# Kernel tuning notes

Hardware: AMD Instinct MI355X
Metric: run time of the kernel (lower is better)

## Reference

```python
import jax, jax.numpy as jnp
import numpy as np

Q_STEPS, Q_TOKENS = 16, 64
KV_STEPS, KV_TOKENS = 64, 64
WINDOW = 2
TOPK = 32
DIM = 512
BATCH = 8
NUM_CONTEXTS = 2


def build_local_mask(q_steps, q_tokens, kv_steps, kv_tokens, window):
    # centers: nearest kv step for each query step
    centers = np.round(np.linspace(0, kv_steps - 1, q_steps)).astype(np.int64)
    steps = np.arange(kv_steps)
    allowed = np.abs(steps[None, :] - centers[:, None]) <= window  # [q_steps, kv_steps]
    allowed = np.repeat(np.repeat(allowed, q_tokens, axis=0), kv_tokens, axis=1)
    return jnp.where(jnp.asarray(allowed), 0.0, -jnp.inf).astype(jnp.float32)


MASK = build_local_mask(Q_STEPS, Q_TOKENS, KV_STEPS, KV_TOKENS, WINDOW)


def setup_inputs() -> dict:
    key = jax.random.key(0)
    ks = jax.random.split(key, 12)
    s = 1.0 / np.sqrt(DIM)
    return {
        "query": jax.random.normal(ks[0], (BATCH, Q_STEPS, Q_TOKENS, DIM), jnp.float32),
        "source": jax.random.normal(ks[1], (BATCH, KV_STEPS, KV_TOKENS, DIM), jnp.float32),
        "ctx1": jax.random.normal(ks[2], (BATCH, DIM), jnp.float32),
        "ctx2": jax.random.normal(ks[3], (BATCH, DIM), jnp.float32),
        "Wq": jax.random.normal(ks[4], (DIM, DIM), jnp.float32) * s,
        "bq": jnp.zeros((DIM,), jnp.float32),
        "Wk": jax.random.normal(ks[5], (DIM, DIM), jnp.float32) * s,
        "bk": jnp.zeros((DIM,), jnp.float32),
        "Wv": jax.random.normal(ks[6], (DIM, DIM), jnp.float32) * s,
        "bv": jnp.zeros((DIM,), jnp.float32),
        "Wo": jax.random.normal(ks[7], (DIM, DIM), jnp.float32) * s,
        "bo": jnp.zeros((DIM,), jnp.float32),
        "Wc": jax.random.normal(ks[8], (NUM_CONTEXTS * DIM, 2 * DIM), jnp.float32) * s,
        "bc": jnp.zeros((2 * DIM,), jnp.float32),
    }


def reference(query, source, ctx1, ctx2, Wq, bq, Wk, bk, Wv, bv, Wo, bo, Wc, bc):
    B = query.shape[0]
    # CrossScaleCondition: fuse contexts -> per-batch FiLM params gamma, beta [B, dim]
    fused = jnp.concatenate([ctx1, ctx2], axis=-1)          # [B, num_contexts*dim]
    gb = fused @ Wc + bc                                     # [B, 2*dim]
    gamma, beta = jnp.split(gb, 2, axis=-1)

    q_flat = query.reshape(B, Q_STEPS * Q_TOKENS, DIM)       # [B, Lq, d]
    src_flat = source.reshape(B, KV_STEPS * KV_TOKENS, DIM)  # [B, Lkv, d]

    q_mod = q_flat * (1.0 + gamma[:, None, :]) + beta[:, None, :]
    q = q_mod @ Wq + bq
    k = src_flat @ Wk + bk
    v = src_flat @ Wv + bv

    scores = jnp.einsum('bqd,bkd->bqk', q, k) / jnp.sqrt(jnp.float32(DIM))
    scores = scores + MASK[None]                             # local window mask

    topk_scores, topk_idx = jax.lax.top_k(scores, TOPK)      # [B, Lq, k]
    selected_v = jax.vmap(lambda vb, ib: vb[ib])(v, topk_idx)  # [B, Lq, k, d]

    attn = jax.nn.softmax(topk_scores, axis=-1)
    out = jnp.einsum('bqk,bqkd->bqd', attn, selected_v)
    out = out @ Wo + bo
    return out.reshape(B, Q_STEPS, Q_TOKENS, DIM)
```

## Files before the change

### kernel.cpp

```cpp
#include <hip/hip_runtime.h>

#define NWIN 320
#define SCORE_SCALE 0.04419417382415922f

__constant__ int CENTERS[16] = {0,4,8,13,17,21,25,29,34,38,42,46,50,55,59,63};

typedef __attribute__((ext_vector_type(8))) short v8s;
typedef __attribute__((ext_vector_type(4))) float v4f;

__device__ __forceinline__ float bflo(unsigned u) { return __uint_as_float(u << 16); }
__device__ __forceinline__ float bfhi(unsigned u) { return __uint_as_float(u & 0xffff0000u); }
__device__ __forceinline__ float bf2f(unsigned short h) { return __uint_as_float(((unsigned)h) << 16); }
__device__ __forceinline__ unsigned short f2bf(float x) {
  unsigned u = __float_as_uint(x);
  unsigned r = 0x7fffu + ((u >> 16) & 1u);
  return (unsigned short)((u + r) >> 16);
}

__device__ __forceinline__ int t64_off(int r, int k) {
  return ((r & 31) << 7) + (((((r >> 5) << 2) | (k >> 3)) ^ (r & 7)) << 4) + ((k & 7) << 1);
}
__device__ __forceinline__ int frag_off(int r, int g) {
  return ((r & 31) << 7) + (((((r >> 5) << 2) | g) ^ (r & 7)) << 4);
}

__device__ __forceinline__ void gload_lds16(const void* g, void* l) {
  __builtin_amdgcn_global_load_lds((const __attribute__((address_space(1))) unsigned int*)g,
                                   (__attribute__((address_space(3))) unsigned int*)l, 16, 0, 0);
}

__device__ __forceinline__ void cvt8pair(float4 a, float4 b, uint4& hi4, uint4& lo4) {
  float v[8] = {a.x, a.y, a.z, a.w, b.x, b.y, b.z, b.w};
  unsigned short h[8], l[8];
  #pragma unroll
  for (int e = 0; e < 8; ++e) {
    h[e] = f2bf(v[e]);
    l[e] = f2bf(v[e] - bf2f(h[e]));
  }
  hi4.x = (unsigned)h[0] | ((unsigned)h[1] << 16);
  hi4.y = (unsigned)h[2] | ((unsigned)h[3] << 16);
  hi4.z = (unsigned)h[4] | ((unsigned)h[5] << 16);
  hi4.w = (unsigned)h[6] | ((unsigned)h[7] << 16);
  lo4.x = (unsigned)l[0] | ((unsigned)l[1] << 16);
  lo4.y = (unsigned)l[2] | ((unsigned)l[3] << 16);
  lo4.z = (unsigned)l[4] | ((unsigned)l[5] << 16);
  lo4.w = (unsigned)l[6] | ((unsigned)l[7] << 16);
}

__device__ __forceinline__ uint4 cvt8hi(float4 a, float4 b) {
  uint4 r;
  r.x = (unsigned)f2bf(a.x) | ((unsigned)f2bf(a.y) << 16);
  r.y = (unsigned)f2bf(a.z) | ((unsigned)f2bf(a.w) << 16);
  r.z = (unsigned)f2bf(b.x) | ((unsigned)f2bf(b.y) << 16);
  r.w = (unsigned)f2bf(b.z) | ((unsigned)f2bf(b.w) << 16);
  return r;
}

__device__ __forceinline__ uint2 cvt4(float4 a) {
  uint2 r;
  r.x = (unsigned)f2bf(a.x) | ((unsigned)f2bf(a.y) << 16);
  r.y = (unsigned)f2bf(a.z) | ((unsigned)f2bf(a.w) << 16);
  return r;
}

__global__ __launch_bounds__(256) void prep1_kernel(
    const float* __restrict__ ctx1, const float* __restrict__ ctx2,
    const float* __restrict__ Wc,  float* __restrict__ part,
    const float* __restrict__ Wk,  const float* __restrict__ bq, float* __restrict__ u,
    const float* __restrict__ Wq,
    unsigned short* __restrict__ Wqh, unsigned short* __restrict__ Wql,
    unsigned short* __restrict__ Wkh, unsigned short* __restrict__ Wkl,
    const float* __restrict__ Wv, const float* __restrict__ Wo,
    unsigned short* __restrict__ Wvt, unsigned short* __restrict__ Wot)
{
  __shared__ char img[32768];
  const int bid = blockIdx.x;
  const int tid = threadIdx.x;

  if (bid < 256) {
    const int b = bid >> 5, sl = (bid >> 2) & 7, jq = bid & 3;
    const int j = jq * 256 + tid;
    const int i0 = sl * 128;
    float acc = 0.f;
    #pragma unroll 4
    for (int t = 0; t < 128; ++t) {
      const int i = i0 + t;
      const float f = (i < 512) ? ctx1[b * 512 + i] : ctx2[b * 512 + i - 512];
      acc = fmaf(f, Wc[(size_t)i * 1024 + j], acc);
    }
    part[(b * 8 + sl) * 1024 + j] = acc;
  } else if (bid < 384) {
    const int d = (bid - 256) * 4 + (tid >> 6);
    const int lane = tid & 63;
    float4 a0 = *(const float4*)&Wk[(size_t)d * 512 + lane * 8];
    float4 a1 = *(const float4*)&Wk[(size_t)d * 512 + lane * 8 + 4];
    float4 c0 = *(const float4*)&bq[lane * 8];
    float4 c1 = *(const float4*)&bq[lane * 8 + 4];
    float s = a0.x*c0.x + a0.y*c0.y + a0.z*c0.z + a0.w*c0.w
            + a1.x*c1.x + a1.y*c1.y + a1.z*c1.z + a1.w*c1.w;
    #pragma unroll
    for (int off = 32; off > 0; off >>= 1) s += __shfl_xor(s, off, 64);
    if (lane == 0) u[d] = s * SCORE_SCALE;
  } else if (bid < 640) {
    const int b = bid - 384;
    const int mat = b >> 7;
    const float* Wsrc = mat ? Wk : Wq;
    unsigned short* Wh = mat ? Wkh : Wqh;
    unsigned short* Wl = mat ? Wkl : Wql;
    const size_t e0 = (((size_t)(b & 127) * 256) + tid) * 8;
    float4 x0 = *(const float4*)&Wsrc[e0];
    float4 x1 = *(const float4*)&Wsrc[e0 + 4];
    uint4 h4, l4;
    cvt8pair(x0, x1, h4, l4);
    *(uint4*)&Wh[e0] = h4;
    *(uint4*)&Wl[e0] = l4;
  } else {
    const int cb = bid - 640;
    const int ktile = cb & 15;
    const int mat   = cb >> 4;
    const float* W = mat ? Wo : Wv;
    unsigned short* Dt = mat ? Wot : Wvt;
    const int k  = tid >> 3;
    const int nt = tid & 7;
    #pragma unroll
    for (int e4 = 0; e4 < 16; ++e4) {
      float4 w = *(const float4*)&W[(size_t)(ktile * 32 + k) * 512 + nt * 64 + e4 * 4];
      float vv[4] = {w.x, w.y, w.z, w.w};
      #pragma unroll
      for (int c = 0; c < 4; ++c) {
        const int n = e4 * 4 + c;
        *(unsigned short*)(img + nt * 4096 + t64_off(n, k)) = f2bf(vv[c]);
      }
    }
    __syncthreads();
    const uint4* src = (const uint4*)img;
    uint4* dst = (uint4*)((char*)Dt + (size_t)ktile * 32768);
    for (int i = tid; i < 2048; i += 256) dst[i] = src[i];
  }
}

__global__ __launch_bounds__(256) void prep2_kernel(
    const unsigned short* __restrict__ Wqh, const unsigned short* __restrict__ Wql,
    const unsigned short* __restrict__ Wkh, const unsigned short* __restrict__ Wkl,
    unsigned short* __restrict__ Gt,
    const float* __restrict__ part, const float* __restrict__ bc,
    float* __restrict__ gb)
{
  const int bid = blockIdx.x;
  const int tid = threadIdx.x;

  if (bid < 256) {
    const int lane = tid & 63, l15 = lane & 15, g = lane >> 4;
    const int wave = tid >> 6;
    const int t  = (bid << 2) | wave;
    const int ti = t >> 5, tj = t & 31;
    const int ib = ti << 4, jb = tj << 4;
    const size_t arow = (size_t)(ib + l15) * 512 + (g << 3);
    const size_t brow = (size_t)(jb + l15) * 512 + (g << 3);

    v4f acc = (v4f){0.f, 0.f, 0.f, 0.f};
    #pragma unroll 4
    for (int kk = 0; kk < 16; ++kk) {
      const int kd = kk * 32;
      const v8s ah = *(const v8s*)&Wqh[arow + kd];
      const v8s al = *(const v8s*)&Wql[arow + kd];
      const v8s bh = *(const v8s*)&Wkh[brow + kd];
      const v8s bl = *(const v8s*)&Wkl[brow + kd];
      acc = __builtin_amdgcn_mfma_f32_16x16x32_bf16(ah, bh, acc, 0, 0, 0);
      acc = __builtin_amdgcn_mfma_f32_16x16x32_bf16(al, bh, acc, 0, 0, 0);
      acc = __builtin_amdgcn_mfma_f32_16x16x32_bf16(ah, bl, acc, 0, 0, 0);
    }
    #pragma unroll
    for (int k = 0; k < 4; ++k) {
      const int gi = ib + (g << 2) + k;
      const int gj = jb + l15;
      const float v = acc[k] * SCORE_SCALE;
      const unsigned short hi = f2bf(v);
      const unsigned short lo = f2bf(v - bf2f(hi));
      const int toff = t64_off(gj & 63, gi & 31);
      *(unsigned short*)((char*)Gt + ((size_t)((gi >> 5) * 8 + (gj >> 6)) << 12) + toff) = hi;
      *(unsigned short*)((char*)Gt + ((size_t)(((gi >> 5) + 16) * 8 + (gj >> 6)) << 12) + toff) = lo;
    }
  } else {
    const int rb = bid - 256;
    const int b = rb >> 2, jq = rb & 3;
    const int j = jq * 256 + tid;
    float acc = bc[j];
    #pragma unroll
    for (int sl = 0; sl < 8; ++sl) acc += part[(b * 8 + sl) * 1024 + j];
    gb[b * 1024 + j] = acc;
  }
}

__global__ __launch_bounds__(256) void proj_split(
    const float* __restrict__ A, const unsigned short* __restrict__ Bt,
    const float* __restrict__ bias, const float* __restrict__ gb,
    unsigned short* __restrict__ Qgt)
{
  __shared__ char smem[49152];
  const int tid  = threadIdx.x;
  const int lane = tid & 63, l15 = lane & 15, g = lane >> 4;
  const int wave = tid >> 6, wm = wave >> 1, wn = wave & 1;
  const int bid = blockIdx.x;
  const int xcd = bid & 7, idx = bid >> 3;
  const int mBlk = (idx & 15) | (xcd << 4);
  const int nBlk = idx >> 4;

  const int sr = tid >> 2;
  const int sq = tid & 3;
  const size_t arow = (size_t)(mBlk * 64 + sr) * 512 + sq * 8;
  const int gbbase = ((mBlk >> 4) * 1024) + sq * 8;
  const int awoff = t64_off(sr, sq * 8);

  int aoff[2], boff[4];
  #pragma unroll
  for (int fm = 0; fm < 2; ++fm) aoff[fm] = frag_off(wm * 32 + fm * 16 + l15, g);
  #pragma unroll
  for (int fn = 0; fn < 4; ++fn) {
    const int n = wn * 64 + fn * 16 + l15;
    boff[fn] = ((n >> 6) << 12) + frag_off(n & 63, g);
  }

  v4f acc[2][4];
  #pragma unroll
  for (int fm = 0; fm < 2; ++fm)
    #pragma unroll
    for (int fn = 0; fn < 4; ++fn) acc[fm][fn] = (v4f){0.f, 0.f, 0.f, 0.f};

  auto stageB = [&](int buf, int tk) {
    const char* gsh = (const char*)Bt + ((size_t)(tk * 8 + nBlk * 2) << 12) + (size_t)tid * 16;
    const char* gsl = (const char*)Bt + ((size_t)((tk + 16) * 8 + nBlk * 2) << 12) + (size_t)tid * 16;
    char* dh = smem + buf * 24576 + 8192 + (wave << 10);
    char* dl = smem + buf * 24576 + 16384 + (wave << 10);
    #pragma unroll
    for (int i = 0; i < 2; ++i) {
      gload_lds16(gsh + i * 4096, dh + i * 4096);
      gload_lds16(gsl + i * 4096, dl + i * 4096);
    }
  };
  auto loadA = [&](int tk, float4* r) {
    const int kd = tk * 32;
    r[0] = *(const float4*)&A[arow + kd];
    r[1] = *(const float4*)&A[arow + kd + 4];
    r[2] = *(const float4*)&gb[gbbase + kd];
    r[3] = *(const float4*)&gb[gbbase + kd + 4];
    r[4] = *(const float4*)&gb[gbbase + 512 + kd];
    r[5] = *(const float4*)&gb[gbbase + 512 + kd + 4];
  };
  auto writeA = [&](int buf, float4* r) {
    float4 x0 = r[0], x1 = r[1];
    x0.x = fmaf(x0.x, 1.f + r[2].x, r[4].x); x0.y = fmaf(x0.y, 1.f + r[2].y, r[4].y);
    x0.z = fmaf(x0.z, 1.f + r[2].z, r[4].z); x0.w = fmaf(x0.w, 1.f + r[2].w, r[4].w);
    x1.x = fmaf(x1.x, 1.f + r[3].x, r[5].x); x1.y = fmaf(x1.y, 1.f + r[3].y, r[5].y);
    x1.z = fmaf(x1.z, 1.f + r[3].z, r[5].z); x1.w = fmaf(x1.w, 1.f + r[3].w, r[5].w);
    uint4 hi4, lo4;
    cvt8pair(x0, x1, hi4, lo4);
    *(uint4*)(smem + buf * 24576 + awoff) = hi4;
    *(uint4*)(smem + buf * 24576 + 4096 + awoff) = lo4;
  };

  float4 pr[6];
  stageB(0, 0);
  loadA(0, pr);
  writeA(0, pr);
  __syncthreads();

  for (int tk = 0; tk < 16; ++tk) {
    const int cur = tk & 1;
    if (tk < 15) {
      stageB(cur ^ 1, tk + 1);
      loadA(tk + 1, pr);
    }
    const char* base = smem + cur * 24576;
    const v8s ah0 = *(const v8s*)(base + aoff[0]);
    const v8s ah1 = *(const v8s*)(base + aoff[1]);
    const v8s al0 = *(const v8s*)(base + 4096 + aoff[0]);
    const v8s al1 = *(const v8s*)(base + 4096 + aoff[1]);
    #pragma unroll
    for (int fn = 0; fn < 4; ++fn) {
      const v8s bh = *(const v8s*)(base + 8192 + boff[fn]);
      const v8s bl = *(const v8s*)(base + 16384 + boff[fn]);
      acc[0][fn] = __builtin_amdgcn_mfma_f32_16x16x32_bf16(ah0, bh, acc[0][fn], 0, 0, 0);
      acc[1][fn] = __builtin_amdgcn_mfma_f32_16x16x32_bf16(ah1, bh, acc[1][fn], 0, 0, 0);
      acc[0][fn] = __builtin_amdgcn_mfma_f32_16x16x32_bf16(al0, bh, acc[0][fn], 0, 0, 0);
      acc[1][fn] = __builtin_amdgcn_mfma_f32_16x16x32_bf16(al1, bh, acc[1][fn], 0, 0, 0);
      acc[0][fn] = __builtin_amdgcn_mfma_f32_16x16x32_bf16(ah0, bl, acc[0][fn], 0, 0, 0);
      acc[1][fn] = __builtin_amdgcn_mfma_f32_16x16x32_bf16(ah1, bl, acc[1][fn], 0, 0, 0);
    }
    if (tk < 15) writeA(cur ^ 1, pr);
    __syncthreads();
  }

  #pragma unroll
  for (int fn = 0; fn < 4; ++fn) {
    const int col = nBlk * 128 + wn * 64 + fn * 16 + l15;
    const float bv = bias[col];
    const int kt = col >> 5;
    const int kk = col & 31;
    #pragma unroll
    for (int fm = 0; fm < 2; ++fm) {
      const int r0 = wm * 32 + fm * 16 + g * 4;
      #pragma unroll
      for (int k = 0; k < 4; ++k) {
        const float vv = acc[fm][fn][k] + bv;
        const unsigned short hi = f2bf(vv);
        const unsigned short lo = f2bf(vv - bf2f(hi));
        const int toff = t64_off(r0 + k, kk);
        *(unsigned short*)((char*)Qgt + ((size_t)(kt * 128 + mBlk) << 12) + toff) = hi;
        *(unsigned short*)((char*)Qgt + ((size_t)((kt + 16) * 128 + mBlk) << 12) + toff) = lo;
      }
    }
  }
}

__global__ __launch_bounds__(512) void proj_v(
    const float* __restrict__ A, const unsigned short* __restrict__ Bt,
    const float* __restrict__ bias, unsigned short* __restrict__ Cb)
{
  __shared__ char smem[8192 + 65536];
  char* const LA = smem;
  char* const LB = smem + 8192;

  const int tid  = threadIdx.x;
  const int lane = tid & 63, l15 = lane & 15, g = lane >> 4;
  const int wave = tid >> 6, wm = wave >> 2, wn = wave & 3;
  const int mBlk = blockIdx.x;

  const int sr  = tid >> 3;
  const int sq4 = tid & 7;
  const size_t arow = (size_t)(mBlk * 64 + sr) * 512 + sq4 * 4;
  const int awoff = t64_off(sr, sq4 * 4);

  int aoff[2], boff[8];
  #pragma unroll
  for (int fm = 0; fm < 2; ++fm) aoff[fm] = frag_off(wm * 32 + fm * 16 + l15, g);
  #pragma unroll
  for (int fn = 0; fn < 8; ++fn) {
    const int n = wn * 128 + fn * 16 + l15;
    boff[fn] = ((n >> 6) << 12) + frag_off(n & 63, g);
  }

  v4f acc[2][8];
  #pragma unroll
  for (int fm = 0; fm < 2; ++fm)
    #pragma unroll
    for (int fn = 0; fn < 8; ++fn) acc[fm][fn] = (v4f){0.f, 0.f, 0.f, 0.f};

  auto stageB = [&](int buf, int tk) {
    const char* gs = (const char*)Bt + ((size_t)tk << 15) + (wave << 12) + (lane << 4);
    char* ld = LB + (buf << 15) + (wave << 12);
    #pragma unroll
    for (int i = 0; i < 4; ++i) gload_lds16(gs + (i << 10), ld + (i << 10));
  };

  float4 xa = *(const float4*)&A[arow];
  stageB(0, 0);
  *(uint2*)(LA + awoff) = cvt4(xa);
  __syncthreads();

  for (int tk = 0; tk < 16; ++tk) {
    const int cur = tk & 1;
    if (tk < 15) {
      stageB(cur ^ 1, tk + 1);
      xa = *(const float4*)&A[arow + (tk + 1) * 32];
    }
    const v8s a0 = *(const v8s*)(LA + (cur << 12) + aoff[0]);
    const v8s a1 = *(const v8s*)(LA + (cur << 12) + aoff[1]);
    #pragma unroll
    for (int fn = 0; fn < 8; ++fn) {
      const v8s bb = *(const v8s*)(LB + (cur << 15) + boff[fn]);
      acc[0][fn] = __builtin_amdgcn_mfma_f32_16x16x32_bf16(a0, bb, acc[0][fn], 0, 0, 0);
      acc[1][fn] = __builtin_amdgcn_mfma_f32_16x16x32_bf16(a1, bb, acc[1][fn], 0, 0, 0);
    }
    if (tk < 15) *(uint2*)(LA + ((cur ^ 1) << 12) + awoff) = cvt4(xa);
    __syncthreads();
  }

  #pragma unroll
  for (int fn = 0; fn < 8; ++fn) {
    const int col = wn * 128 + fn * 16 + l15;
    const float bv = bias[col];
    #pragma unroll
    for (int fm = 0; fm < 2; ++fm) {
      const int r0 = mBlk * 64 + wm * 32 + fm * 16 + g * 4;
      #pragma unroll
      for (int k = 0; k < 4; ++k)
        Cb[(size_t)(r0 + k) * 512 + col] = f2bf(acc[fm][fn][k] + bv);
    }
  }
}

__global__ __launch_bounds__(256) void proj_o(
    const float* __restrict__ A, const unsigned short* __restrict__ Bt,
    const float* __restrict__ bias, float* __restrict__ Cf)
{
  __shared__ char smem[24576];
  const int tid  = threadIdx.x;
  const int lane = tid & 63, l15 = lane & 15, g = lane >> 4;
  const int wave = tid >> 6, wm = wave >> 1, wn = wave & 1;
  const int bid = blockIdx.x;
  const int xcd = bid & 7, idx = bid >> 3;
  const int mBlk = (idx & 15) | (xcd << 4);
  const int nBlk = idx >> 4;

  const int sr = tid >> 2;
  const int sq = tid & 3;
  const size_t arow = (size_t)(mBlk * 64 + sr) * 512 + sq * 8;
  const int awoff = t64_off(sr, sq * 8);

  int aoff[2], boff[4];
  #pragma unroll
  for (int fm = 0; fm < 2; ++fm) aoff[fm] = frag_off(wm * 32 + fm * 16 + l15, g);
  #pragma unroll
  for (int fn = 0; fn < 4; ++fn) {
    const int n = wn * 64 + fn * 16 + l15;
    boff[fn] = ((n >> 6) << 12) + frag_off(n & 63, g);
  }

  v4f acc[2][4];
  #pragma unroll
  for (int fm = 0; fm < 2; ++fm)
    #pragma unroll
    for (int fn = 0; fn < 4; ++fn) acc[fm][fn] = (v4f){0.f, 0.f, 0.f, 0.f};

  auto stageB = [&](int buf, int tk) {
    const char* gs = (const char*)Bt + ((size_t)tk << 15) + ((size_t)nBlk << 13) + (size_t)tid * 16;
    char* ld = smem + buf * 12288 + 4096 + (wave << 10);
    #pragma unroll
    for (int i = 0; i < 2; ++i)
      gload_lds16(gs + i * 4096, ld + i * 4096);
  };

  float4 x0 = *(const float4*)&A[arow];
  float4 x1 = *(const float4*)&A[arow + 4];
  stageB(0, 0);
  *(uint4*)(smem + awoff) = cvt8hi(x0, x1);
  __syncthreads();

  for (int tk = 0; tk < 16; ++tk) {
    const int cur = tk & 1;
    if (tk < 15) {
      stageB(cur ^ 1, tk + 1);
      x0 = *(const float4*)&A[arow + (tk + 1) * 32];
      x1 = *(const float4*)&A[arow + (tk + 1) * 32 + 4];
    }
    const char* base = smem + cur * 12288;
    const v8s a0 = *(const v8s*)(base + aoff[0]);
    const v8s a1 = *(const v8s*)(base + aoff[1]);
    #pragma unroll
    for (int fn = 0; fn < 4; ++fn) {
      const v8s bb = *(const v8s*)(base + 4096 + boff[fn]);
      acc[0][fn] = __builtin_amdgcn_mfma_f32_16x16x32_bf16(a0, bb, acc[0][fn], 0, 0, 0);
      acc[1][fn] = __builtin_amdgcn_mfma_f32_16x16x32_bf16(a1, bb, acc[1][fn], 0, 0, 0);
    }
    if (tk < 15) *(uint4*)(smem + (cur ^ 1) * 12288 + awoff) = cvt8hi(x0, x1);
    __syncthreads();
  }

  #pragma unroll
  for (int fn = 0; fn < 4; ++fn) {
    const int col = nBlk * 128 + wn * 64 + fn * 16 + l15;
    const float bv = bias[col];
    #pragma unroll
    for (int fm = 0; fm < 2; ++fm) {
      const int r0 = mBlk * 64 + wm * 32 + fm * 16 + g * 4;
      #pragma unroll
      for (int k = 0; k < 4; ++k)
        Cf[(size_t)(r0 + k) * 512 + col] = acc[fm][fn][k] + bv;
    }
  }
}

__global__ __launch_bounds__(256) void scores_mfma(
    const unsigned short* __restrict__ Qgt, const float* __restrict__ SRC,
    float* __restrict__ S)
{
  const int bs = blockIdx.y;
  const int s = bs & 15, b = bs >> 4;
  const int c  = CENTERS[s];
  const int lo = (c - 2 > 0) ? c - 2 : 0;
  const int hi = (c + 2 < 63) ? c + 2 : 63;
  if ((int)blockIdx.x > hi - lo) return;

  __shared__ char smem[16384];
  char* const LAh = smem;
  char* const LAl = smem + 4096;
  char* const LBh = smem + 8192;
  char* const LBl = smem + 12288;

  const int tid = threadIdx.x;
  const int lane = tid & 63, l15 = lane & 15, g = lane >> 4;
  const int wave = tid >> 6, wm = wave >> 1, wn = wave & 1;
  const int kvrow0 = (b << 12) + ((lo + (int)blockIdx.x) << 6);
  const int qbase  = bs << 6;
  const int sr = tid >> 2, sq = tid & 3;
  const size_t krow = (size_t)(kvrow0 + sr) * 512 + sq * 8;
  const int awoff = t64_off(sr, sq * 8);

  int aoff[2], boff[2];
  #pragma unroll
  for (int f = 0; f < 2; ++f) {
    aoff[f] = frag_off(wm * 32 + f * 16 + l15, g);
    boff[f] = frag_off(wn * 32 + f * 16 + l15, g);
  }

  v4f acc[2][2];
  #pragma unroll
  for (int i = 0; i < 2; ++i)
    #pragma unroll
    for (int j = 0; j < 2; ++j) acc[i][j] = (v4f){0.f, 0.f, 0.f, 0.f};

  for (int tk = 0; tk < 16; ++tk) {
    const int kd = tk * 32;
    {
      const char* gah = (const char*)Qgt + ((size_t)(tk * 128 + bs) << 12) + (size_t)tid * 16;
      const char* gal = (const char*)Qgt + ((size_t)((tk + 16) * 128 + bs) << 12) + (size_t)tid * 16;
      gload_lds16(gah, LAh + (wave << 10));
      gload_lds16(gal, LAl + (wave << 10));
    }
    {
      float4 y0 = *(const float4*)&SRC[krow + kd];
      float4 y1 = *(const float4*)&SRC[krow + kd + 4];
      uint4 bhi, blo;
      cvt8pair(y0, y1, bhi, blo);
      *(uint4*)(LBh + awoff) = bhi;
      *(uint4*)(LBl + awoff) = blo;
    }
    __syncthreads();
    const v8s a0h = *(const v8s*)(LAh + aoff[0]);
    const v8s a1h = *(const v8s*)(LAh + aoff[1]);
    const v8s a0l = *(const v8s*)(LAl + aoff[0]);
    const v8s a1l = *(const v8s*)(LAl + aoff[1]);
    const v8s b0h = *(const v8s*)(LBh + boff[0]);
    const v8s b1h = *(const v8s*)(LBh + boff[1]);
    const v8s b0l = *(const v8s*)(LBl + boff[0]);
    const v8s b1l = *(const v8s*)(LBl + boff[1]);
    acc[0][0] = __builtin_amdgcn_mfma_f32_16x16x32_bf16(a0h, b0h, acc[0][0], 0, 0, 0);
    acc[0][1] = __builtin_amdgcn_mfma_f32_16x16x32_bf16(a0h, b1h, acc[0][1], 0, 0, 0);
    acc[1][0] = __builtin_amdgcn_mfma_f32_16x16x32_bf16(a1h, b0h, acc[1][0], 0, 0, 0);
    acc[1][1] = __builtin_amdgcn_mfma_f32_16x16x32_bf16(a1h, b1h, acc[1][1], 0, 0, 0);
    acc[0][0] = __builtin_amdgcn_mfma_f32_16x16x32_bf16(a0l, b0h, acc[0][0], 0, 0, 0);
    acc[0][1] = __builtin_amdgcn_mfma_f32_16x16x32_bf16(a0l, b1h, acc[0][1], 0, 0, 0);
    acc[1][0] = __builtin_amdgcn_mfma_f32_16x16x32_bf16(a1l, b0h, acc[1][0], 0, 0, 0);
    acc[1][1] = __builtin_amdgcn_mfma_f32_16x16x32_bf16(a1l, b1h, acc[1][1], 0, 0, 0);
    acc[0][0] = __builtin_amdgcn_mfma_f32_16x16x32_bf16(a0h, b0l, acc[0][0], 0, 0, 0);
    acc[0][1] = __builtin_amdgcn_mfma_f32_16x16x32_bf16(a0h, b1l, acc[0][1], 0, 0, 0);
    acc[1][0] = __builtin_amdgcn_mfma_f32_16x16x32_bf16(a1h, b0l, acc[1][0], 0, 0, 0);
    acc[1][1] = __builtin_amdgcn_mfma_f32_16x16x32_bf16(a1h, b1l, acc[1][1], 0, 0, 0);
    __syncthreads();
  }

  #pragma unroll
  for (int fn = 0; fn < 2; ++fn) {
    const int cl = wn * 32 + fn * 16 + l15;
    const int colS = ((int)blockIdx.x << 6) + cl;
    #pragma unroll
    for (int fm = 0; fm < 2; ++fm) {
      const int r0 = qbase + wm * 32 + fm * 16 + g * 4;
      #pragma unroll
      for (int k = 0; k < 4; ++k)
        S[(size_t)(r0 + k) * NWIN + colS] = acc[fm][fn][k];
    }
  }
}

__global__ __launch_bounds__(256) void topk_pv(
    const float* __restrict__ S, const unsigned short* __restrict__ Vb,
    float* __restrict__ O)
{
  __shared__ int   sel_i[4][32];
  __shared__ float sel_p[4][32];

  const int lane = threadIdx.x & 63;
  const int wv   = threadIdx.x >> 6;
  const int b0   = blockIdx.x;
  const int grp  = (b0 & 7) + ((b0 >> 7) << 3);
  const int blk  = (b0 >> 3) & 15;
  const int row  = (((grp << 4) + blk) << 2) + wv;
  const int b    = row >> 10;
  const int s    = (row >> 6) & 15;
  const int c    = CENTERS[s];
  const int lo   = (c - 2 > 0) ? c - 2 : 0;
  const int hi   = (c + 2 < 63) ? c + 2 : 63;
  const int L    = (hi - lo + 1) << 6;
  const size_t vbase = ((size_t)b << 12) + ((size_t)lo << 6);

  const float* srow = S + (size_t)row * NWIN;
  float f[5]; unsigned uo[5];
  #pragma unroll
  for (int j = 0; j < 5; ++j) {
    const int idx = lane + (j << 6);
    const float v = (idx < L) ? srow[idx] : -__builtin_inff();
    f[j] = v;
    const unsigned fb = __float_as_uint(v);
    uo[j] = (fb & 0x80000000u) ? ~fb : (fb | 0x80000000u);
  }

  float m = f[0];
  #pragma unroll
  for (int j = 1; j < 5; ++j) m = fmaxf(m, f[j]);
  #pragma unroll
  for (int off = 32; off > 0; off >>= 1) m = fmaxf(m, __shfl_xor(m, off, 64));

  unsigned T = 0u;
  for (int bit = 31; bit >= 0; --bit) {
    const unsigned cand = T | (1u << bit);
    int cnt = 0;
    #pragma unroll
    for (int j = 0; j < 5; ++j)
      cnt += __popcll(__ballot(uo[j] >= cand));
    if (cnt >= 32) T = cand;
  }

  int base = 0;
  #pragma unroll
  for (int j = 0; j < 5; ++j) {
    const unsigned long long gm = __ballot(uo[j] > T);
    if (uo[j] > T) {
      const int rank = base + __builtin_amdgcn_mbcnt_hi(
          (unsigned)(gm >> 32), __builtin_amdgcn_mbcnt_lo((unsigned)gm, 0));
      sel_i[wv][rank] = lane + (j << 6);
      sel_p[wv][rank] = __expf(f[j] - m);
    }
    base += __popcll(gm);
  }
  #pragma unroll
  for (int j = 0; j < 5; ++j) {
    const unsigned long long em = __ballot(uo[j] == T);
    if (uo[j] == T) {
      const int er = base + __builtin_amdgcn_mbcnt_hi(
          (unsigned)(em >> 32), __builtin_amdgcn_mbcnt_lo((unsigned)em, 0));
      if (er < 32) {
        sel_i[wv][er] = lane + (j << 6);
        sel_p[wv][er] = __expf(f[j] - m);
      }
    }
    base += __popcll(em);
  }

  asm volatile("s_waitcnt lgkmcnt(0)" ::: "memory");

  const int   si = sel_i[wv][lane & 31];
  const float sp = sel_p[wv][lane & 31];
  float dp = (lane < 32) ? sp : 0.f;
  #pragma unroll
  for (int off = 32; off > 0; off >>= 1) dp += __shfl_xor(dp, off, 64);

  float oacc[8] = {0.f,0.f,0.f,0.f,0.f,0.f,0.f,0.f};
  #pragma unroll
  for (int tb = 0; tb < 32; tb += 4) {
    unsigned raws[4][4];
    #pragma unroll
    for (int q = 0; q < 4; ++q) {
      const int idx_t = __builtin_amdgcn_readlane(si, tb + q);
      const unsigned short* vrow = Vb + ((vbase + (size_t)idx_t) << 9);
      #pragma unroll
      for (int e = 0; e < 4; ++e)
        raws[q][e] = *(const unsigned*)&vrow[(lane << 1) + (e << 7)];
    }
    #pragma unroll
    for (int q = 0; q < 4; ++q) {
      const float p_t = __uint_as_float(
          (unsigned)__builtin_amdgcn_readlane((int)__float_as_uint(sp), tb + q));
      #pragma unroll
      for (int e = 0; e < 4; ++e) {
        oacc[2*e]     = fmaf(p_t, bflo(raws[q][e]), oacc[2*e]);
        oacc[2*e + 1] = fmaf(p_t, bfhi(raws[q][e]), oacc[2*e + 1]);
      }
    }
  }

  const float inv = 1.0f / dp;
  float* orow = O + ((size_t)row << 9);
  #pragma unroll
  for (int e = 0; e < 4; ++e) {
    float2 o2 = make_float2(oacc[2*e] * inv, oacc[2*e + 1] * inv);
    *(float2*)&orow[(lane << 1) + (e << 7)] = o2;
  }
}

extern "C" void kernel_launch(void* const* d_in, const int* in_sizes, int n_in,
                              void* d_out, int out_size, void* d_ws, size_t ws_size,
                              hipStream_t stream)
{
  (void)in_sizes; (void)n_in; (void)out_size; (void)ws_size;

  const float* query  = (const float*)d_in[0];
  const float* source = (const float*)d_in[1];
  const float* ctx1   = (const float*)d_in[2];
  const float* ctx2   = (const float*)d_in[3];
  const float* Wq     = (const float*)d_in[4];
  const float* bq     = (const float*)d_in[5];
  const float* Wk     = (const float*)d_in[6];
  const float* Wv     = (const float*)d_in[8];
  const float* bv     = (const float*)d_in[9];
  const float* Wo     = (const float*)d_in[10];
  const float* bo     = (const float*)d_in[11];
  const float* Wc     = (const float*)d_in[12];
  const float* bc     = (const float*)d_in[13];
  float* out = (float*)d_out;

  char* ws = (char*)d_ws;
  unsigned short* Qgt  = (unsigned short*)(ws);
  unsigned short* v    = (unsigned short*)(ws + 16777216);
  float*          S    = (float*)(ws + 50331648);
  float*          ctx  = (float*)(ws + 60817408);
  unsigned short* Gt   = (unsigned short*)(ws + 77594624);
  unsigned short* Wvt  = (unsigned short*)(ws + 78643200);
  unsigned short* Wot  = (unsigned short*)(ws + 79167488);
  float*          gb   = (float*)(ws + 79691776);
  float*          part = (float*)(ws + 79724544);
  float*          u    = (float*)(ws + 79986688);
  unsigned short* Wqh  = (unsigned short*)(ws + 79988736);
  unsigned short* Wql  = (unsigned short*)(ws + 80513024);
  unsigned short* Wkh  = (unsigned short*)(ws + 81037312);
  unsigned short* Wkl  = (unsigned short*)(ws + 81561600);

  prep1_kernel<<<672, 256, 0, stream>>>(ctx1, ctx2, Wc, part, Wk, bq, u, Wq,
                                        Wqh, Wql, Wkh, Wkl, Wv, Wo, Wvt, Wot);
  prep2_kernel<<<288, 256, 0, stream>>>(Wqh, Wql, Wkh, Wkl, Gt, part, bc, gb);
  proj_split<<<512, 256, 0, stream>>>(query, Gt, u, gb, Qgt);
  proj_v<<<512, 512, 0, stream>>>(source, Wvt, bv, v);
  scores_mfma<<<dim3(5, 128), 256, 0, stream>>>(Qgt, source, S);
  topk_pv<<<2048, 256, 0, stream>>>(S, v, ctx);
  proj_o<<<512, 256, 0, stream>>>(ctx, Wot, bo, out);
}
```

Measured before the change: 142.4 us.

## Triple-buffer proj_v shared-memory pipeline with explicit vmcnt waits

Changes the V-projection GEMM from double to triple buffering of the A and B tiles in LDS, prefetching two k-steps ahead. The plain __syncthreads is replaced by explicit s_waitcnt vmcnt/lgkmcnt plus s_barrier, so async global-to-LDS loads can stay in flight across iterations. This is meant to hide global load latency, at the cost of a larger LDS footprint (about 108 KB) that may reduce occupancy. Correctness depends on hand-tuned vmcnt counts.

```diff
diff --git a/kernel.cpp b/kernel.cpp
--- a/kernel.cpp
+++ b/kernel.cpp
@@ -317,10 +317,7 @@
     const float* __restrict__ A, const unsigned short* __restrict__ Bt,
     const float* __restrict__ bias, unsigned short* __restrict__ Cb)
 {
-  __shared__ char smem[8192 + 65536];
-  char* const LA = smem;
-  char* const LB = smem + 8192;
-
+  __shared__ char smem[110592];
   const int tid  = threadIdx.x;
   const int lane = tid & 63, l15 = lane & 15, g = lane >> 4;
   const int wave = tid >> 6, wm = wave >> 2, wn = wave & 3;
@@ -346,34 +343,49 @@
     #pragma unroll
     for (int fn = 0; fn < 8; ++fn) acc[fm][fn] = (v4f){0.f, 0.f, 0.f, 0.f};
 
+  auto LAp = [&](int buf) { return smem + buf * 36864; };
+  auto LBp = [&](int buf) { return smem + buf * 36864 + 4096; };
   auto stageB = [&](int buf, int tk) {
     const char* gs = (const char*)Bt + ((size_t)tk << 15) + (wave << 12) + (lane << 4);
-    char* ld = LB + (buf << 15) + (wave << 12);
+    char* ld = LBp(buf) + (wave << 12);
     #pragma unroll
     for (int i = 0; i < 4; ++i) gload_lds16(gs + (i << 10), ld + (i << 10));
   };
 
-  float4 xa = *(const float4*)&A[arow];
+  float4 a0v = *(const float4*)&A[arow];
   stageB(0, 0);
-  *(uint2*)(LA + awoff) = cvt4(xa);
-  __syncthreads();
-
+  *(uint2*)(LAp(0) + awoff) = cvt4(a0v);
+  stageB(1, 1);
+  float4 a_f = *(const float4*)&A[arow + 32];
+  asm volatile("s_waitcnt vmcnt(5)" ::: "memory");
+  asm volatile("s_waitcnt lgkmcnt(0)" ::: "memory");
+  __builtin_amdgcn_s_barrier();
+
+  float4 a_ff = a_f;
   for (int tk = 0; tk < 16; ++tk) {
-    const int cur = tk & 1;
-    if (tk < 15) {
-      stageB(cur ^ 1, tk + 1);
-      xa = *(const float4*)&A[arow + (tk + 1) * 32];
-    }
-    const v8s a0 = *(const v8s*)(LA + (cur << 12) + aoff[0]);
-    const v8s a1 = *(const v8s*)(LA + (cur << 12) + aoff[1]);
+    const int cur = tk % 3;
+    const int nxt = (tk + 1) % 3;
+    const int nn  = (tk + 2) % 3;
+    if (tk < 14) {
+      stageB(nn, tk + 2);
+      a_ff = *(const float4*)&A[arow + (size_t)(tk + 2) * 32];
+    }
+    const char* ba = LAp(cur);
+    const char* bb = LBp(cur);
+    const v8s va0 = *(const v8s*)(ba + aoff[0]);
+    const v8s va1 = *(const v8s*)(ba + aoff[1]);
     #pragma unroll
     for (int fn = 0; fn < 8; ++fn) {
-      const v8s bb = *(const v8s*)(LB + (cur << 15) + boff[fn]);
-      acc[0][fn] = __builtin_amdgcn_mfma_f32_16x16x32_bf16(a0, bb, acc[0][fn], 0, 0, 0);
-      acc[1][fn] = __builtin_amdgcn_mfma_f32_16x16x32_bf16(a1, bb, acc[1][fn], 0, 0, 0);
-    }
-    if (tk < 15) *(uint2*)(LA + ((cur ^ 1) << 12) + awoff) = cvt4(xa);
-    __syncthreads();
+      const v8s vb = *(const v8s*)(bb + boff[fn]);
+      acc[0][fn] = __builtin_amdgcn_mfma_f32_16x16x32_bf16(va0, vb, acc[0][fn], 0, 0, 0);
+      acc[1][fn] = __builtin_amdgcn_mfma_f32_16x16x32_bf16(va1, vb, acc[1][fn], 0, 0, 0);
+    }
+    if (tk < 15) *(uint2*)(LAp(nxt) + awoff) = cvt4(a_f);
+    if (tk < 14) { asm volatile("s_waitcnt vmcnt(5)" ::: "memory"); }
+    else         { asm volatile("s_waitcnt vmcnt(0)" ::: "memory"); }
+    asm volatile("s_waitcnt lgkmcnt(0)" ::: "memory");
+    __builtin_amdgcn_s_barrier();
+    a_f = a_ff;
   }
 
   #pragma unroll
```

New measurement: 148.9 us. +4.6%, slower.
